# Performance work log

Hardware: AMD Instinct MI355X
Metric: run time of the kernel (lower is better)

The kernel has to match this reference:

```python
import jax, jax.numpy as jnp
import numpy as np

B, S, HID = 4, 4096, 1024
H, D = 16, 64  # num_head, attn_dim
EPS = 1e-6


def setup_inputs() -> dict:
    key = jax.random.key(0)
    ks = jax.random.split(key, 9)
    sc = 1.0 / np.sqrt(HID)
    return {
        "x": jax.random.normal(ks[0], (B, S, HID), jnp.float32),
        "Wq": jax.random.normal(ks[1], (HID, H * D), jnp.float32) * sc,
        "bq": jnp.zeros((H * D,), jnp.float32),
        "Wk": jax.random.normal(ks[2], (HID, H * D), jnp.float32) * sc,
        "bk": jnp.zeros((H * D,), jnp.float32),
        "Wv": jax.random.normal(ks[3], (HID, H * D), jnp.float32) * sc,
        "bv": jnp.zeros((H * D,), jnp.float32),
        "Wo": jax.random.normal(ks[4], (H * D, HID), jnp.float32) * sc,
        "bo": jnp.zeros((HID,), jnp.float32),
    }


def _phi(x):
    # feature_map == 'elu': elu(x) + 1
    return jax.nn.elu(x) + 1.0


def reference(x, Wq, bq, Wk, bk, Wv, bv, Wo, bo):
    bs, n, _ = x.shape
    # projections -> [b, n, h, d], then scan axis first -> [n, b, h, d]
    Q = _phi((x @ Wq + bq).reshape(bs, n, H, D)).transpose(1, 0, 2, 3)
    K = _phi((x @ Wk + bk).reshape(bs, n, H, D)).transpose(1, 0, 2, 3)
    V = (x @ Wv + bv).reshape(bs, n, H, D).transpose(1, 0, 2, 3)

    KV0 = jnp.zeros((bs, H, D, D), x.dtype)
    Ks0 = jnp.zeros((bs, H, D), x.dtype)

    def step(carry, qkv):
        KV, Ks = carry
        qi, ki, vi = qkv  # each [b, h, d]
        KV = KV + jnp.einsum('bhd,bhe->bhde', ki, vi)
        Ks = Ks + ki
        num = jnp.einsum('bhd,bhde->bhe', qi, KV)
        den = jnp.einsum('bhd,bhd->bh', qi, Ks)
        return (KV, Ks), num / (den[..., None] + EPS)

    _, out = jax.lax.scan(step, (KV0, Ks0), (Q, K, V))  # out: [n, b, h, d]
    out = out.transpose(1, 0, 2, 3).reshape(bs, n, H * D)
    return out @ Wo + bo
```

## Files before the change

kernel.cpp:

```cpp
#include <hip/hip_runtime.h>
#include <stdint.h>


#define DEVI __device__ __forceinline__

typedef __attribute__((ext_vector_type(8))) short bf16x8;
typedef __attribute__((ext_vector_type(4))) float f32x4;
typedef unsigned short u16;

DEVI u16 f2bf(float f) {
  union { float f; uint32_t u; } x; x.f = f;
  return (u16)((x.u + 0x7FFFu + ((x.u >> 16) & 1u)) >> 16);
}
DEVI float bf2f(u16 u) {
  union { uint32_t u; float f; } x; x.u = ((uint32_t)u) << 16;
  return x.f;
}
DEVI f32x4 mfma16(bf16x8 a, bf16x8 b, f32x4 c) {
  return __builtin_amdgcn_mfma_f32_16x16x32_bf16(a, b, c, 0, 0, 0);
}

typedef __attribute__((address_space(3))) void* lds_vp;
typedef const __attribute__((address_space(1))) void* glb_vp;
DEVI void gload_lds16(const void* g, void* l) {
  __builtin_amdgcn_global_load_lds((glb_vp)g, (lds_vp)l, 16, 0, 0);
}

static constexpr int Ss  = 4096;
static constexpr int Hh  = 16;
static constexpr int CC  = 64;
static constexpr int NCC = Ss / CC;

__global__ __launch_bounds__(256) void cvt_bf16_k(const float* __restrict__ in,
                                                  u16* __restrict__ out, int n8) {
  const int i = blockIdx.x * 256 + threadIdx.x;
  if (i >= n8) return;
  const float4* p = (const float4*)(in + (size_t)i * 8);
  const float4 a = p[0], b = p[1];
  union { uint4 v; u16 s[8]; } u;
  u.s[0] = f2bf(a.x); u.s[1] = f2bf(a.y); u.s[2] = f2bf(a.z); u.s[3] = f2bf(a.w);
  u.s[4] = f2bf(b.x); u.s[5] = f2bf(b.y); u.s[6] = f2bf(b.z); u.s[7] = f2bf(b.w);
  ((uint4*)out)[i] = u.v;
}

__global__ __launch_bounds__(256) void transpose_cvt_k(const float* __restrict__ in,
                                                       u16* __restrict__ out) {
  __shared__ float tl[32][33];
  const int tx = threadIdx.x & 31, ty = threadIdx.x >> 5;
  const int bx = blockIdx.x, by = blockIdx.y;
#pragma unroll
  for (int j = 0; j < 4; ++j)
    tl[ty + j * 8][tx] = in[(size_t)(by * 32 + ty + j * 8) * 1024 + bx * 32 + tx];
  __syncthreads();
#pragma unroll
  for (int j = 0; j < 4; ++j)
    out[(size_t)(bx * 32 + ty + j * 8) * 1024 + by * 32 + tx] = f2bf(tl[tx][ty + j * 8]);
}

template <bool FUSED, bool OUTF32>
__global__ __launch_bounds__(512, 2) void gemm256_k(const u16* __restrict__ A,
                                                    const u16* __restrict__ BT,
                                                    const float* __restrict__ b0,
                                                    const float* __restrict__ b1,
                                                    const float* __restrict__ b2,
                                                    void* __restrict__ out,
                                                    int M, int K) {
  __shared__ __attribute__((aligned(16))) u16 lds[65536];
  const int t = threadIdx.x, lane = t & 63, w = t >> 6;
  const int wm = w >> 2, wn = w & 3;

  const int nx = gridDim.x;
  const int nwg = nx * gridDim.y;
  const int bid = blockIdx.y * nx + blockIdx.x;
  const int swz = (bid & 7) * (nwg >> 3) + (bid >> 3);
  const int bx = swz % nx, by = swz / nx;
  const int m0 = by * 256, n0 = bx * 256;

  const u16* gA = A + (size_t)m0 * K;
  const u16* gB = BT + (size_t)n0 * K;

  const int sr = t >> 2;
  const int sc = (t & 3) ^ ((sr >> 1) & 3);
  auto stage = [&](const u16* gm, u16* dst, int kof) {
    gload_lds16(gm + (size_t)sr * K + kof + sc * 8, dst + t * 8);
    gload_lds16(gm + (size_t)(sr + 128) * K + kof + sc * 8, dst + 4096 + t * 8);
  };

  f32x4 acc[8][4];
#pragma unroll
  for (int i = 0; i < 8; ++i)
#pragma unroll
    for (int j = 0; j < 4; ++j) acc[i][j] = f32x4{0.f, 0.f, 0.f, 0.f};

  stage(gA, lds, 0);          stage(gB, lds + 32768, 0);
  stage(gA, lds + 8192, 32);  stage(gB, lds + 40960, 32);

  const int fr = lane & 15, kq = lane >> 4;
  const int rdko = ((kq ^ ((fr >> 1) & 3)) << 3);
  const int arow0 = wm * 128 + fr;
  const int brow0 = wn * 64 + fr;

  const int nk = K >> 6;
  for (int kt = 0; kt < nk; ++kt) {
    const int buf = kt & 1;
    u16* Ax = lds + buf * 16384;
    u16* Bx = lds + 32768 + buf * 16384;
    u16* Ay = lds + (buf ^ 1) * 16384;
    u16* By = lds + 32768 + (buf ^ 1) * 16384;
    const bool pf = (kt + 1 < nk);
    const int kon = (kt + 1) << 6;
    bf16x8 af[8], bg0, bg1;

#pragma unroll
    for (int half = 0; half < 2; ++half) {
      u16* Axh = Ax + half * 8192;
      u16* Bxh = Bx + half * 8192;
      if (half == 0 || pf) asm volatile("s_waitcnt vmcnt(4)" ::: "memory");
      else                 asm volatile("s_waitcnt vmcnt(0)" ::: "memory");
      __builtin_amdgcn_s_barrier();
      if (pf) stage(gA, Ay + half * 8192, kon + half * 32);
#pragma unroll
      for (int fi = 0; fi < 8; ++fi)
        af[fi] = *(const bf16x8*)(Axh + (arow0 + fi * 16) * 32 + rdko);
      bg0 = *(const bf16x8*)(Bxh + brow0 * 32 + rdko);
      bg1 = *(const bf16x8*)(Bxh + (brow0 + 16) * 32 + rdko);
      asm volatile("s_waitcnt lgkmcnt(0)" ::: "memory");
      __builtin_amdgcn_sched_barrier(0);
      __builtin_amdgcn_s_setprio(1);
#pragma unroll
      for (int fi = 0; fi < 8; ++fi) {
        acc[fi][0] = mfma16(af[fi], bg0, acc[fi][0]);
        acc[fi][1] = mfma16(af[fi], bg1, acc[fi][1]);
      }
      __builtin_amdgcn_s_setprio(0);
      __builtin_amdgcn_sched_barrier(0);
      if (pf) stage(gB, By + half * 8192, kon + half * 32);
      bg0 = *(const bf16x8*)(Bxh + (brow0 + 32) * 32 + rdko);
      bg1 = *(const bf16x8*)(Bxh + (brow0 + 48) * 32 + rdko);
      asm volatile("s_waitcnt lgkmcnt(0)" ::: "memory");
      __builtin_amdgcn_sched_barrier(0);
      __builtin_amdgcn_s_setprio(1);
#pragma unroll
      for (int fi = 0; fi < 8; ++fi) {
        acc[fi][2] = mfma16(af[fi], bg0, acc[fi][2]);
        acc[fi][3] = mfma16(af[fi], bg1, acc[fi][3]);
      }
      __builtin_amdgcn_s_setprio(0);
      __builtin_amdgcn_sched_barrier(0);
    }
  }

  const int rowg = (lane >> 4) * 4;
  if constexpr (!OUTF32) {
    __syncthreads();
    const int seg  = FUSED ? (n0 >> 10) : 0;
    const int lcol0 = FUSED ? (n0 & 1023) : n0;
    const float* bp = b0;
    if constexpr (FUSED) bp = (seg == 0) ? b0 : (seg == 1) ? b1 : b2;
#pragma unroll
    for (int fj = 0; fj < 4; ++fj) {
      const int col = wn * 64 + fj * 16 + fr;
      const float bv = bp[lcol0 + col];
#pragma unroll
      for (int fi = 0; fi < 8; ++fi) {
#pragma unroll
        for (int rr = 0; rr < 4; ++rr) {
          const int row = wm * 128 + fi * 16 + rowg + rr;
          float v = acc[fi][fj][rr] + bv;
          if (FUSED && seg < 2) v = (v > 0.f) ? (v + 1.f) : __expf(v);
          lds[row * 256 + (((col >> 3) ^ ((row >> 2) & 31)) << 3) + (col & 7)] = f2bf(v);
        }
      }
    }
    __syncthreads();
    u16* outp = (u16*)out + (size_t)seg * M * 1024 + (size_t)m0 * 1024 + lcol0;
#pragma unroll
    for (int it = 0; it < 16; ++it) {
      const int g = it * 512 + t;
      const int row = g >> 5, c16 = g & 31;
      const uint4 v = *(const uint4*)&lds[row * 256 + ((c16 ^ ((row >> 2) & 31)) << 3)];
      *(uint4*)(outp + (size_t)row * 1024 + c16 * 8) = v;
    }
  } else {
    float* flds = (float*)lds;
#pragma unroll
    for (int pass = 0; pass < 2; ++pass) {
      __syncthreads();
      if (wm == pass) {
#pragma unroll
        for (int fj = 0; fj < 4; ++fj) {
          const int col = wn * 64 + fj * 16 + fr;
          const float bv = b0[n0 + col];
#pragma unroll
          for (int fi = 0; fi < 8; ++fi) {
#pragma unroll
            for (int rr = 0; rr < 4; ++rr) {
              const int rl = fi * 16 + rowg + rr;
              flds[rl * 256 + (((col >> 2) ^ ((rl >> 2) & 63)) << 2) + (col & 3)] =
                  acc[fi][fj][rr] + bv;
            }
          }
        }
      }
      __syncthreads();
      float* outp = (float*)out + (size_t)(m0 + pass * 128) * 1024 + n0;
#pragma unroll
      for (int it = 0; it < 16; ++it) {
        const int g = it * 512 + t;
        const int row = g >> 6, c16 = g & 63;
        const uint4 v = *(const uint4*)&flds[row * 256 + ((c16 ^ ((row >> 2) & 63)) << 2)];
        *(uint4*)(outp + (size_t)row * 1024 + c16 * 4) = v;
      }
    }
  }
}

__global__ __launch_bounds__(256) void chunk_kv_k(const u16* __restrict__ Kb,
                                                  const u16* __restrict__ Vb,
                                                  u16* __restrict__ KVTc,
                                                  float* __restrict__ Ksc) {
  const int c = blockIdx.x, h = blockIdx.y, b = blockIdx.z;
  __shared__ u16 KT[64][72], VT[64][72];
  const int t = threadIdx.x, lane = t & 63, w = t >> 6;
  {
    const int i = t >> 2, c0 = (t & 3) * 16;
    const size_t g = ((size_t)(b * Ss + c * CC + i)) * 1024 + h * 64 + c0;
    const u16* kp = Kb + g;
    const u16* vp = Vb + g;
#pragma unroll
    for (int j = 0; j < 16; ++j) { KT[c0 + j][i] = kp[j]; VT[c0 + j][i] = vp[j]; }
  }
  __syncthreads();
  f32x4 acc[4];
#pragma unroll
  for (int j = 0; j < 4; ++j) acc[j] = f32x4{0.f, 0.f, 0.f, 0.f};
  const int fr = lane & 15, kq = (lane >> 4) * 8;
#pragma unroll
  for (int kk = 0; kk < 2; ++kk) {
    const bf16x8 av = *(const bf16x8*)&VT[w * 16 + fr][kk * 32 + kq];
#pragma unroll
    for (int fj = 0; fj < 4; ++fj) {
      const bf16x8 bk = *(const bf16x8*)&KT[fj * 16 + fr][kk * 32 + kq];
      acc[fj] = mfma16(av, bk, acc[fj]);
    }
  }
  const size_t base = ((size_t)((b * Hh + h) * NCC + c)) * 4096;
#pragma unroll
  for (int fj = 0; fj < 4; ++fj)
#pragma unroll
    for (int rr = 0; rr < 4; ++rr) {
      const int e = w * 16 + (lane >> 4) * 4 + rr;
      const int d = fj * 16 + fr;
      KVTc[base + (size_t)e * 64 + d] = f2bf(acc[fj][rr]);
    }
  if (t < 64) {
    float s = 0.f;
#pragma unroll
    for (int ii = 0; ii < 8; ++ii) {
      const bf16x8 kv = *(const bf16x8*)&KT[t][ii * 8];
#pragma unroll
      for (int j = 0; j < 8; ++j) s += bf2f((u16)kv[j]);
    }
    Ksc[((size_t)((b * Hh + h) * NCC + c)) * 64 + t] = s;
  }
}

__global__ __launch_bounds__(256) void prefix_k(const u16* __restrict__ KVTc,
                                                const float* __restrict__ Ksc,
                                                u16* __restrict__ KVpreT,
                                                float* __restrict__ Kspre) {
  const int bh = blockIdx.x, eg = blockIdx.y;
  const int t = threadIdx.x;
  const int e4 = eg * 1024 + t * 4;
  const u16* src = KVTc + (size_t)bh * NCC * 4096 + e4;
  u16* dst = KVpreT + (size_t)bh * NCC * 4096 + e4;
  const float* kss = Ksc + (size_t)bh * NCC * 64 + t;
  float* ksd = Kspre + (size_t)bh * NCC * 64 + t;
  float run[4] = {0.f, 0.f, 0.f, 0.f};
  float rk = 0.f;
  for (int c = 0; c < NCC; ++c) {
    union { uint2 v; u16 s[4]; } in, ov;
    in.v = *(const uint2*)(src + (size_t)c * 4096);
#pragma unroll
    for (int j = 0; j < 4; ++j) { ov.s[j] = f2bf(run[j]); run[j] += bf2f(in.s[j]); }
    *(uint2*)(dst + (size_t)c * 4096) = ov.v;
    if (eg == 0 && t < 64) { ksd[(size_t)c * 64] = rk; rk += kss[(size_t)c * 64]; }
  }
}

__global__ __launch_bounds__(256) void chunk_out_k(const u16* __restrict__ Qb,
                                                   const u16* __restrict__ Kb,
                                                   const u16* __restrict__ Vb,
                                                   const u16* __restrict__ KVpreT,
                                                   const float* __restrict__ Kspre,
                                                   u16* __restrict__ attn) {
  const int c = blockIdx.x, h = blockIdx.y, b = blockIdx.z;
  const int bh = b * Hh + h;
  __shared__ u16 Ql[64][72], Kl[64][72], VT[64][72], Pl[64][72];
  __shared__ float den[64];
  const int t = threadIdx.x, lane = t & 63, w = t >> 6;

  {
    const int i = t >> 2, c0 = (t & 3) * 16;
    const size_t g = ((size_t)(b * Ss + c * CC + i)) * 1024 + h * 64 + c0;
    const uint4* qp = (const uint4*)(Qb + g);
    uint4* qd = (uint4*)&Ql[i][c0]; qd[0] = qp[0]; qd[1] = qp[1];
    const uint4* kp = (const uint4*)(Kb + g);
    uint4* kd = (uint4*)&Kl[i][c0]; kd[0] = kp[0]; kd[1] = kp[1];
    const u16* vp = Vb + g;
#pragma unroll
    for (int j = 0; j < 16; ++j) VT[c0 + j][i] = vp[j];
  }
  __syncthreads();

  f32x4 sacc[4];
#pragma unroll
  for (int fj = 0; fj < 4; ++fj) sacc[fj] = f32x4{0.f, 0.f, 0.f, 0.f};
#pragma unroll
  for (int kd = 0; kd < 2; ++kd) {
    const bf16x8 aq = *(const bf16x8*)&Ql[w * 16 + (lane & 15)][kd * 32 + (lane >> 4) * 8];
#pragma unroll
    for (int fj = 0; fj < 4; ++fj) {
      const bf16x8 bk = *(const bf16x8*)&Kl[fj * 16 + (lane & 15)][kd * 32 + (lane >> 4) * 8];
      sacc[fj] = mfma16(aq, bk, sacc[fj]);
    }
  }
  float rowsum[4] = {0.f, 0.f, 0.f, 0.f};
#pragma unroll
  for (int fj = 0; fj < 4; ++fj) {
#pragma unroll
    for (int rr = 0; rr < 4; ++rr) {
      const int i_loc = w * 16 + (lane >> 4) * 4 + rr;
      const int j_loc = fj * 16 + (lane & 15);
      const float v = (j_loc <= i_loc) ? sacc[fj][rr] : 0.f;
      Pl[i_loc][j_loc] = f2bf(v);
      rowsum[rr] += v;
    }
  }
#pragma unroll
  for (int off = 1; off < 16; off <<= 1) {
#pragma unroll
    for (int rr = 0; rr < 4; ++rr) rowsum[rr] += __shfl_xor(rowsum[rr], off, 64);
  }
  if ((lane & 15) == 0) {
#pragma unroll
    for (int rr = 0; rr < 4; ++rr) den[w * 16 + (lane >> 4) * 4 + rr] = rowsum[rr];
  }
  __syncthreads();
  {
    const int i = t >> 2, part = t & 3;
    const float* ksp = Kspre + ((size_t)(bh * NCC + c)) * 64 + part * 16;
    float s = 0.f;
#pragma unroll
    for (int sg = 0; sg < 2; ++sg) {
      const bf16x8 q = *(const bf16x8*)&Ql[i][part * 16 + sg * 8];
#pragma unroll
      for (int j = 0; j < 8; ++j) s += bf2f((u16)q[j]) * ksp[sg * 8 + j];
    }
    s += __shfl_xor(s, 1, 64);
    s += __shfl_xor(s, 2, 64);
    if (part == 0) den[i] = den[i] + s + 1e-6f;
  }
  __syncthreads();

  f32x4 oacc[4];
#pragma unroll
  for (int fj = 0; fj < 4; ++fj) oacc[fj] = f32x4{0.f, 0.f, 0.f, 0.f};
  const u16* kvb = KVpreT + ((size_t)(bh * NCC + c)) * 4096;
#pragma unroll
  for (int ks2 = 0; ks2 < 2; ++ks2) {
    const bf16x8 aq = *(const bf16x8*)&Ql[w * 16 + (lane & 15)][ks2 * 32 + (lane >> 4) * 8];
#pragma unroll
    for (int fj = 0; fj < 4; ++fj) {
      const bf16x8 bv =
          *(const bf16x8*)(kvb + (size_t)(fj * 16 + (lane & 15)) * 64 + ks2 * 32 + (lane >> 4) * 8);
      oacc[fj] = mfma16(aq, bv, oacc[fj]);
    }
  }
#pragma unroll
  for (int ks3 = 0; ks3 < 2; ++ks3) {
    const bf16x8 ap = *(const bf16x8*)&Pl[w * 16 + (lane & 15)][ks3 * 32 + (lane >> 4) * 8];
#pragma unroll
    for (int fj = 0; fj < 4; ++fj) {
      const bf16x8 bv = *(const bf16x8*)&VT[fj * 16 + (lane & 15)][ks3 * 32 + (lane >> 4) * 8];
      oacc[fj] = mfma16(ap, bv, oacc[fj]);
    }
  }
#pragma unroll
  for (int fj = 0; fj < 4; ++fj) {
#pragma unroll
    for (int rr = 0; rr < 4; ++rr) {
      const int i_loc = w * 16 + (lane >> 4) * 4 + rr;
      const int e = fj * 16 + (lane & 15);
      const float v = oacc[fj][rr] / den[i_loc];
      attn[((size_t)(b * Ss + c * CC + i_loc)) * 1024 + h * 64 + e] = f2bf(v);
    }
  }
}

extern "C" void kernel_launch(void* const* d_in, const int* in_sizes, int n_in,
                              void* d_out, int out_size, void* d_ws, size_t ws_size,
                              hipStream_t stream) {
  (void)in_sizes; (void)n_in; (void)out_size; (void)ws_size;
  const float* x  = (const float*)d_in[0];
  const float* Wq = (const float*)d_in[1];
  const float* bq = (const float*)d_in[2];
  const float* Wk = (const float*)d_in[3];
  const float* bk = (const float*)d_in[4];
  const float* Wv = (const float*)d_in[5];
  const float* bv = (const float*)d_in[6];
  const float* Wo = (const float*)d_in[7];
  const float* bo = (const float*)d_in[8];
  float* out = (float*)d_out;
  char* ws = (char*)d_ws;

  size_t off = 0;
  auto take = [&](size_t bytes) { size_t r = off; off += (bytes + 255) & ~(size_t)255; return r; };
  const size_t WQKV_B = (size_t)3072 * 1024 * 2;
  const size_t WT_B   = (size_t)1024 * 1024 * 2;
  const size_t BIG_B  = (size_t)16384 * 1024 * 2;
  const size_t KVT_B  = (size_t)64 * NCC * 4096 * 2;
  const size_t KS_B   = (size_t)64 * NCC * 64 * 4;

  u16* WqkvT  = (u16*)(ws + take(WQKV_B));
  u16* WoT    = (u16*)(ws + take(WT_B));
  size_t shared_off = take(BIG_B);
  u16* xbf    = (u16*)(ws + shared_off);
  u16* KVTc   = (u16*)(ws + shared_off);
  u16* attn   = (u16*)(ws + shared_off);
  u16* Qb     = (u16*)(ws + take(BIG_B));
  u16* Kb     = (u16*)(ws + take(BIG_B));
  u16* Vb     = (u16*)(ws + take(BIG_B));
  u16* KVpreT = (u16*)(ws + take(KVT_B));
  float* Ksc  = (float*)(ws + take(KS_B));
  float* Kspre= (float*)(ws + take(KS_B));

  const dim3 blk(256);
  cvt_bf16_k<<<dim3(8192), blk, 0, stream>>>(x, xbf, 16384 * 1024 / 8);
  const dim3 gT(32, 32);
  transpose_cvt_k<<<gT, blk, 0, stream>>>(Wq, WqkvT);
  transpose_cvt_k<<<gT, blk, 0, stream>>>(Wk, WqkvT + (size_t)1024 * 1024);
  transpose_cvt_k<<<gT, blk, 0, stream>>>(Wv, WqkvT + (size_t)2048 * 1024);
  transpose_cvt_k<<<gT, blk, 0, stream>>>(Wo, WoT);

  gemm256_k<true, false><<<dim3(12, 64), dim3(512), 0, stream>>>(
      xbf, WqkvT, bq, bk, bv, Qb, 16384, 1024);

  const dim3 gC(NCC, Hh, 4);
  chunk_kv_k<<<gC, blk, 0, stream>>>(Kb, Vb, KVTc, Ksc);
  prefix_k<<<dim3(64, 4), blk, 0, stream>>>(KVTc, Ksc, KVpreT, Kspre);
  chunk_out_k<<<gC, blk, 0, stream>>>(Qb, Kb, Vb, KVpreT, Kspre, attn);

  gemm256_k<false, true><<<dim3(4, 64), dim3(512), 0, stream>>>(
      attn, WoT, bo, NULL, NULL, out, 16384, 1024);
}
```

Before: 267.4 us.

## Restructure GEMM barrier/prefetch schedule and merge four weight-transpose launches

```diff
diff --git a/kernel.cpp b/kernel.cpp
--- a/kernel.cpp
+++ b/kernel.cpp
@@ -25,6 +25,10 @@
 DEVI void gload_lds16(const void* g, void* l) {
   __builtin_amdgcn_global_load_lds((glb_vp)g, (lds_vp)l, 16, 0, 0);
 }
+
+#define BAR()   asm volatile("s_barrier" ::: "memory")
+#define LGKM0() do { asm volatile("s_waitcnt lgkmcnt(0)" ::: "memory"); \
+                     __builtin_amdgcn_sched_barrier(0); } while (0)
 
 static constexpr int Ss  = 4096;
 static constexpr int Hh  = 16;
@@ -43,9 +47,16 @@
   ((uint4*)out)[i] = u.v;
 }
 
-__global__ __launch_bounds__(256) void transpose_cvt_k(const float* __restrict__ in,
-                                                       u16* __restrict__ out) {
+__global__ __launch_bounds__(256) void transpose_cvt4_k(const float* __restrict__ w0,
+                                                        const float* __restrict__ w1,
+                                                        const float* __restrict__ w2,
+                                                        const float* __restrict__ w3,
+                                                        u16* __restrict__ dqkv,
+                                                        u16* __restrict__ dwo) {
   __shared__ float tl[32][33];
+  const int z = blockIdx.z;
+  const float* in = (z == 0) ? w0 : (z == 1) ? w1 : (z == 2) ? w2 : w3;
+  u16* out = (z < 3) ? (dqkv + (size_t)z * 1024 * 1024) : dwo;
   const int tx = threadIdx.x & 31, ty = threadIdx.x >> 5;
   const int bx = blockIdx.x, by = blockIdx.y;
 #pragma unroll
@@ -94,6 +105,8 @@
 
   stage(gA, lds, 0);          stage(gB, lds + 32768, 0);
   stage(gA, lds + 8192, 32);  stage(gB, lds + 40960, 32);
+  asm volatile("s_waitcnt vmcnt(4)" ::: "memory");
+  BAR();
 
   const int fr = lane & 15, kq = lane >> 4;
   const int rdko = ((kq ^ ((fr >> 1) & 3)) << 3);
@@ -102,30 +115,26 @@
 
   const int nk = K >> 6;
   for (int kt = 0; kt < nk; ++kt) {
-    const int buf = kt & 1;
-    u16* Ax = lds + buf * 16384;
-    u16* Bx = lds + 32768 + buf * 16384;
-    u16* Ay = lds + (buf ^ 1) * 16384;
-    u16* By = lds + 32768 + (buf ^ 1) * 16384;
+    const int d = kt & 1;
     const bool pf = (kt + 1 < nk);
     const int kon = (kt + 1) << 6;
+    u16* Ac = lds + d * 16384;
+    u16* Bc = lds + 32768 + d * 16384;
+    u16* An = lds + (d ^ 1) * 16384;
+    u16* Bn = lds + 32768 + (d ^ 1) * 16384;
     bf16x8 af[8], bg0, bg1;
-
-#pragma unroll
-    for (int half = 0; half < 2; ++half) {
-      u16* Axh = Ax + half * 8192;
-      u16* Bxh = Bx + half * 8192;
-      if (half == 0 || pf) asm volatile("s_waitcnt vmcnt(4)" ::: "memory");
-      else                 asm volatile("s_waitcnt vmcnt(0)" ::: "memory");
-      __builtin_amdgcn_s_barrier();
-      if (pf) stage(gA, Ay + half * 8192, kon + half * 32);
+#pragma unroll
+    for (int h = 0; h < 2; ++h) {
+      const u16* Ah = Ac + h * 8192;
+      const u16* Bh = Bc + h * 8192;
 #pragma unroll
       for (int fi = 0; fi < 8; ++fi)
-        af[fi] = *(const bf16x8*)(Axh + (arow0 + fi * 16) * 32 + rdko);
-      bg0 = *(const bf16x8*)(Bxh + brow0 * 32 + rdko);
-      bg1 = *(const bf16x8*)(Bxh + (brow0 + 16) * 32 + rdko);
-      asm volatile("s_waitcnt lgkmcnt(0)" ::: "memory");
-      __builtin_amdgcn_sched_barrier(0);
+        af[fi] = *(const bf16x8*)(Ah + (arow0 + fi * 16) * 32 + rdko);
+      bg0 = *(const bf16x8*)(Bh + brow0 * 32 + rdko);
+      bg1 = *(const bf16x8*)(Bh + (brow0 + 16) * 32 + rdko);
+      if (pf) stage(gA, An + h * 8192, kon + h * 32);
+      BAR();
+      LGKM0();
       __builtin_amdgcn_s_setprio(1);
 #pragma unroll
       for (int fi = 0; fi < 8; ++fi) {
@@ -134,11 +143,12 @@
       }
       __builtin_amdgcn_s_setprio(0);
       __builtin_amdgcn_sched_barrier(0);
-      if (pf) stage(gB, By + half * 8192, kon + half * 32);
-      bg0 = *(const bf16x8*)(Bxh + (brow0 + 32) * 32 + rdko);
-      bg1 = *(const bf16x8*)(Bxh + (brow0 + 48) * 32 + rdko);
-      asm volatile("s_waitcnt lgkmcnt(0)" ::: "memory");
-      __builtin_amdgcn_sched_barrier(0);
+      BAR();
+      bg0 = *(const bf16x8*)(Bh + (brow0 + 32) * 32 + rdko);
+      bg1 = *(const bf16x8*)(Bh + (brow0 + 48) * 32 + rdko);
+      if (pf) stage(gB, Bn + h * 8192, kon + h * 32);
+      BAR();
+      LGKM0();
       __builtin_amdgcn_s_setprio(1);
 #pragma unroll
       for (int fi = 0; fi < 8; ++fi) {
@@ -147,6 +157,13 @@
       }
       __builtin_amdgcn_s_setprio(0);
       __builtin_amdgcn_sched_barrier(0);
+      if (h == 0) {
+        if (pf) asm volatile("s_waitcnt vmcnt(4)" ::: "memory");
+        else    asm volatile("s_waitcnt vmcnt(0)" ::: "memory");
+      } else if (pf) {
+        asm volatile("s_waitcnt vmcnt(4)" ::: "memory");
+      }
+      BAR();
     }
   }
 
@@ -437,11 +454,7 @@
 
   const dim3 blk(256);
   cvt_bf16_k<<<dim3(8192), blk, 0, stream>>>(x, xbf, 16384 * 1024 / 8);
-  const dim3 gT(32, 32);
-  transpose_cvt_k<<<gT, blk, 0, stream>>>(Wq, WqkvT);
-  transpose_cvt_k<<<gT, blk, 0, stream>>>(Wk, WqkvT + (size_t)1024 * 1024);
-  transpose_cvt_k<<<gT, blk, 0, stream>>>(Wv, WqkvT + (size_t)2048 * 1024);
-  transpose_cvt_k<<<gT, blk, 0, stream>>>(Wo, WoT);
+  transpose_cvt4_k<<<dim3(32, 32, 4), blk, 0, stream>>>(Wq, Wk, Wv, Wo, WqkvT, WoT);
 
   gemm256_k<true, false><<<dim3(12, 64), dim3(512), 0, stream>>>(
       xbf, WqkvT, bq, bk, bv, Qb, 16384, 1024);
```

New measurement: 266.3 us. No clear change (-0.4%).

## Fuse chunked linear attention into one sequential-scan kernel per head slice

Applied to the files above, without the earlier changes.

```diff
diff --git a/kernel.cpp b/kernel.cpp
--- a/kernel.cpp
+++ b/kernel.cpp
@@ -25,6 +25,9 @@
 DEVI void gload_lds16(const void* g, void* l) {
   __builtin_amdgcn_global_load_lds((glb_vp)g, (lds_vp)l, 16, 0, 0);
 }
+
+#define LGKM_BAR() do { asm volatile("s_waitcnt lgkmcnt(0)" ::: "memory"); \
+                        __builtin_amdgcn_s_barrier(); } while (0)
 
 static constexpr int Ss  = 4096;
 static constexpr int Hh  = 16;
@@ -43,9 +46,16 @@
   ((uint4*)out)[i] = u.v;
 }
 
-__global__ __launch_bounds__(256) void transpose_cvt_k(const float* __restrict__ in,
-                                                       u16* __restrict__ out) {
+__global__ __launch_bounds__(256) void transpose_cvt4_k(const float* __restrict__ w0,
+                                                        const float* __restrict__ w1,
+                                                        const float* __restrict__ w2,
+                                                        const float* __restrict__ w3,
+                                                        u16* __restrict__ dqkv,
+                                                        u16* __restrict__ dwo) {
   __shared__ float tl[32][33];
+  const int z = blockIdx.z;
+  const float* in = (z == 0) ? w0 : (z == 1) ? w1 : (z == 2) ? w2 : w3;
+  u16* out = (z < 3) ? (dqkv + (size_t)z * 1024 * 1024) : dwo;
   const int tx = threadIdx.x & 31, ty = threadIdx.x >> 5;
   const int bx = blockIdx.x, by = blockIdx.y;
 #pragma unroll
@@ -215,186 +225,155 @@
   }
 }
 
-__global__ __launch_bounds__(256) void chunk_kv_k(const u16* __restrict__ Kb,
-                                                  const u16* __restrict__ Vb,
-                                                  u16* __restrict__ KVTc,
-                                                  float* __restrict__ Ksc) {
-  const int c = blockIdx.x, h = blockIdx.y, b = blockIdx.z;
-  __shared__ u16 KT[64][72], VT[64][72];
+__global__ __launch_bounds__(512, 1) void fused_attn_k(const u16* __restrict__ Qb,
+                                                       const u16* __restrict__ Kb,
+                                                       const u16* __restrict__ Vb,
+                                                       u16* __restrict__ attn) {
+  __shared__ __attribute__((aligned(16))) u16 Ql[2][4096];
+  __shared__ u16 Kl[64][72], KTl[64][72];
+  __shared__ u16 VT[16][72], KVbf[16][72];
+  __shared__ u16 Pl[64][72];
+  __shared__ float Ksf[64], ksp[4][64], denp[2][64], den[64];
+
   const int t = threadIdx.x, lane = t & 63, w = t >> 6;
-  {
-    const int i = t >> 2, c0 = (t & 3) * 16;
-    const size_t g = ((size_t)(b * Ss + c * CC + i)) * 1024 + h * 64 + c0;
-    const u16* kp = Kb + g;
-    const u16* vp = Vb + g;
-#pragma unroll
-    for (int j = 0; j < 16; ++j) { KT[c0 + j][i] = kp[j]; VT[c0 + j][i] = vp[j]; }
-  }
-  __syncthreads();
-  f32x4 acc[4];
-#pragma unroll
-  for (int j = 0; j < 4; ++j) acc[j] = f32x4{0.f, 0.f, 0.f, 0.f};
-  const int fr = lane & 15, kq = (lane >> 4) * 8;
-#pragma unroll
-  for (int kk = 0; kk < 2; ++kk) {
-    const bf16x8 av = *(const bf16x8*)&VT[w * 16 + fr][kk * 32 + kq];
-#pragma unroll
-    for (int fj = 0; fj < 4; ++fj) {
-      const bf16x8 bk = *(const bf16x8*)&KT[fj * 16 + fr][kk * 32 + kq];
-      acc[fj] = mfma16(av, bk, acc[fj]);
-    }
-  }
-  const size_t base = ((size_t)((b * Hh + h) * NCC + c)) * 4096;
-#pragma unroll
-  for (int fj = 0; fj < 4; ++fj)
-#pragma unroll
-    for (int rr = 0; rr < 4; ++rr) {
-      const int e = w * 16 + (lane >> 4) * 4 + rr;
-      const int d = fj * 16 + fr;
-      KVTc[base + (size_t)e * 64 + d] = f2bf(acc[fj][rr]);
-    }
-  if (t < 64) {
-    float s = 0.f;
-#pragma unroll
-    for (int ii = 0; ii < 8; ++ii) {
-      const bf16x8 kv = *(const bf16x8*)&KT[t][ii * 8];
-#pragma unroll
-      for (int j = 0; j < 8; ++j) s += bf2f((u16)kv[j]);
-    }
-    Ksc[((size_t)((b * Hh + h) * NCC + c)) * 64 + t] = s;
-  }
-}
-
-__global__ __launch_bounds__(256) void prefix_k(const u16* __restrict__ KVTc,
-                                                const float* __restrict__ Ksc,
-                                                u16* __restrict__ KVpreT,
-                                                float* __restrict__ Kspre) {
-  const int bh = blockIdx.x, eg = blockIdx.y;
-  const int t = threadIdx.x;
-  const int e4 = eg * 1024 + t * 4;
-  const u16* src = KVTc + (size_t)bh * NCC * 4096 + e4;
-  u16* dst = KVpreT + (size_t)bh * NCC * 4096 + e4;
-  const float* kss = Ksc + (size_t)bh * NCC * 64 + t;
-  float* ksd = Kspre + (size_t)bh * NCC * 64 + t;
-  float run[4] = {0.f, 0.f, 0.f, 0.f};
-  float rk = 0.f;
+  const int bid = blockIdx.x;
+  const int g = bid & 7, slot = bid >> 3;
+  const int bh = g * 8 + (slot >> 2), eg = slot & 3;
+  const int b = bh >> 4, h = bh & 15;
+
+  const u16* qbase = Qb + (size_t)(b * Ss) * 1024 + h * 64;
+  const u16* kbase = Kb + (size_t)(b * Ss) * 1024 + h * 64;
+  const u16* vbase = Vb + (size_t)(b * Ss) * 1024 + h * 64 + eg * 16;
+  u16* abase = attn + (size_t)(b * Ss) * 1024 + h * 64 + eg * 16;
+
+  const int qr = t >> 3, qc = t & 7;
+  const int kr = t >> 3, kc8 = (t & 7) * 8;
+  const int vr = t >> 3, vc = (t & 7) * 2;
+  const int fr = lane & 15, kq = lane >> 4;
+
+  auto qstage = [&](int c, int buf) {
+    gload_lds16(qbase + (size_t)(c * 64 + qr) * 1024 + ((qc ^ (qr & 7)) << 3),
+                &Ql[buf][t * 8]);
+  };
+  uint4 kreg; uint32_t vreg;
+  auto kvload = [&](int c) {
+    kreg = *(const uint4*)(kbase + (size_t)(c * 64 + kr) * 1024 + kc8);
+    vreg = *(const uint32_t*)(vbase + (size_t)(c * 64 + vr) * 1024 + vc);
+  };
+
+  f32x4 kvacc = f32x4{0.f, 0.f, 0.f, 0.f};
+  if (t < 64) Ksf[t] = 0.f;
+
+  qstage(0, 0);
+  kvload(0);
+
   for (int c = 0; c < NCC; ++c) {
-    union { uint2 v; u16 s[4]; } in, ov;
-    in.v = *(const uint2*)(src + (size_t)c * 4096);
-#pragma unroll
-    for (int j = 0; j < 4; ++j) { ov.s[j] = f2bf(run[j]); run[j] += bf2f(in.s[j]); }
-    *(uint2*)(dst + (size_t)c * 4096) = ov.v;
-    if (eg == 0 && t < 64) { ksd[(size_t)c * 64] = rk; rk += kss[(size_t)c * 64]; }
-  }
-}
-
-__global__ __launch_bounds__(256) void chunk_out_k(const u16* __restrict__ Qb,
-                                                   const u16* __restrict__ Kb,
-                                                   const u16* __restrict__ Vb,
-                                                   const u16* __restrict__ KVpreT,
-                                                   const float* __restrict__ Kspre,
-                                                   u16* __restrict__ attn) {
-  const int c = blockIdx.x, h = blockIdx.y, b = blockIdx.z;
-  const int bh = b * Hh + h;
-  __shared__ u16 Ql[64][72], Kl[64][72], VT[64][72], Pl[64][72];
-  __shared__ float den[64];
-  const int t = threadIdx.x, lane = t & 63, w = t >> 6;
-
-  {
-    const int i = t >> 2, c0 = (t & 3) * 16;
-    const size_t g = ((size_t)(b * Ss + c * CC + i)) * 1024 + h * 64 + c0;
-    const uint4* qp = (const uint4*)(Qb + g);
-    uint4* qd = (uint4*)&Ql[i][c0]; qd[0] = qp[0]; qd[1] = qp[1];
-    const uint4* kp = (const uint4*)(Kb + g);
-    uint4* kd = (uint4*)&Kl[i][c0]; kd[0] = kp[0]; kd[1] = kp[1];
-    const u16* vp = Vb + g;
-#pragma unroll
-    for (int j = 0; j < 16; ++j) VT[c0 + j][i] = vp[j];
-  }
-  __syncthreads();
-
-  f32x4 sacc[4];
-#pragma unroll
-  for (int fj = 0; fj < 4; ++fj) sacc[fj] = f32x4{0.f, 0.f, 0.f, 0.f};
-#pragma unroll
-  for (int kd = 0; kd < 2; ++kd) {
-    const bf16x8 aq = *(const bf16x8*)&Ql[w * 16 + (lane & 15)][kd * 32 + (lane >> 4) * 8];
-#pragma unroll
-    for (int fj = 0; fj < 4; ++fj) {
-      const bf16x8 bk = *(const bf16x8*)&Kl[fj * 16 + (lane & 15)][kd * 32 + (lane >> 4) * 8];
-      sacc[fj] = mfma16(aq, bk, sacc[fj]);
-    }
-  }
-  float rowsum[4] = {0.f, 0.f, 0.f, 0.f};
-#pragma unroll
-  for (int fj = 0; fj < 4; ++fj) {
-#pragma unroll
-    for (int rr = 0; rr < 4; ++rr) {
-      const int i_loc = w * 16 + (lane >> 4) * 4 + rr;
-      const int j_loc = fj * 16 + (lane & 15);
-      const float v = (j_loc <= i_loc) ? sacc[fj][rr] : 0.f;
-      Pl[i_loc][j_loc] = f2bf(v);
-      rowsum[rr] += v;
-    }
-  }
-#pragma unroll
-  for (int off = 1; off < 16; off <<= 1) {
-#pragma unroll
-    for (int rr = 0; rr < 4; ++rr) rowsum[rr] += __shfl_xor(rowsum[rr], off, 64);
-  }
-  if ((lane & 15) == 0) {
-#pragma unroll
-    for (int rr = 0; rr < 4; ++rr) den[w * 16 + (lane >> 4) * 4 + rr] = rowsum[rr];
-  }
-  __syncthreads();
-  {
-    const int i = t >> 2, part = t & 3;
-    const float* ksp = Kspre + ((size_t)(bh * NCC + c)) * 64 + part * 16;
-    float s = 0.f;
-#pragma unroll
-    for (int sg = 0; sg < 2; ++sg) {
-      const bf16x8 q = *(const bf16x8*)&Ql[i][part * 16 + sg * 8];
-#pragma unroll
-      for (int j = 0; j < 8; ++j) s += bf2f((u16)q[j]) * ksp[sg * 8 + j];
-    }
-    s += __shfl_xor(s, 1, 64);
-    s += __shfl_xor(s, 2, 64);
-    if (part == 0) den[i] = den[i] + s + 1e-6f;
-  }
-  __syncthreads();
-
-  f32x4 oacc[4];
-#pragma unroll
-  for (int fj = 0; fj < 4; ++fj) oacc[fj] = f32x4{0.f, 0.f, 0.f, 0.f};
-  const u16* kvb = KVpreT + ((size_t)(bh * NCC + c)) * 4096;
-#pragma unroll
-  for (int ks2 = 0; ks2 < 2; ++ks2) {
-    const bf16x8 aq = *(const bf16x8*)&Ql[w * 16 + (lane & 15)][ks2 * 32 + (lane >> 4) * 8];
-#pragma unroll
-    for (int fj = 0; fj < 4; ++fj) {
-      const bf16x8 bv =
-          *(const bf16x8*)(kvb + (size_t)(fj * 16 + (lane & 15)) * 64 + ks2 * 32 + (lane >> 4) * 8);
-      oacc[fj] = mfma16(aq, bv, oacc[fj]);
-    }
-  }
-#pragma unroll
-  for (int ks3 = 0; ks3 < 2; ++ks3) {
-    const bf16x8 ap = *(const bf16x8*)&Pl[w * 16 + (lane & 15)][ks3 * 32 + (lane >> 4) * 8];
-#pragma unroll
-    for (int fj = 0; fj < 4; ++fj) {
-      const bf16x8 bv = *(const bf16x8*)&VT[fj * 16 + (lane & 15)][ks3 * 32 + (lane >> 4) * 8];
-      oacc[fj] = mfma16(ap, bv, oacc[fj]);
-    }
-  }
-#pragma unroll
-  for (int fj = 0; fj < 4; ++fj) {
-#pragma unroll
-    for (int rr = 0; rr < 4; ++rr) {
-      const int i_loc = w * 16 + (lane >> 4) * 4 + rr;
-      const int e = fj * 16 + (lane & 15);
-      const float v = oacc[fj][rr] / den[i_loc];
-      attn[((size_t)(b * Ss + c * CC + i_loc)) * 1024 + h * 64 + e] = f2bf(v);
-    }
+    const int buf = c & 1;
+    {
+      union { uint4 v; u16 s[8]; } ku; ku.v = kreg;
+      *(uint4*)&Kl[kr][kc8] = ku.v;
+#pragma unroll
+      for (int j = 0; j < 8; ++j) KTl[kc8 + j][kr] = ku.s[j];
+      union { uint32_t v; u16 s[2]; } vu; vu.v = vreg;
+      VT[vc][vr] = vu.s[0]; VT[vc + 1][vr] = vu.s[1];
+      if (w >= 4) {
+#pragma unroll
+        for (int r = 0; r < 4; ++r)
+          KVbf[(lane >> 4) * 4 + r][(w - 4) * 16 + fr] = f2bf(kvacc[r]);
+      }
+    }
+    if (c + 1 < NCC) { qstage(c + 1, buf ^ 1); kvload(c + 1); }
+    LGKM_BAR();
+
+    const int r0 = (w & 3) * 16;
+    const int ch = w >> 2;
+    f32x4 sacc[2];
+    sacc[0] = f32x4{0.f, 0.f, 0.f, 0.f};
+    sacc[1] = f32x4{0.f, 0.f, 0.f, 0.f};
+#pragma unroll
+    for (int kk = 0; kk < 2; ++kk) {
+      const bf16x8 aq =
+          *(const bf16x8*)&Ql[buf][(r0 + fr) * 64 + (((kk * 4 + kq) ^ (fr & 7)) << 3)];
+#pragma unroll
+      for (int j = 0; j < 2; ++j) {
+        const bf16x8 bk = *(const bf16x8*)&Kl[(ch * 2 + j) * 16 + fr][kk * 32 + kq * 8];
+        sacc[j] = mfma16(aq, bk, sacc[j]);
+      }
+    }
+    float rs[4] = {0.f, 0.f, 0.f, 0.f};
+#pragma unroll
+    for (int j = 0; j < 2; ++j) {
+      const int colb = (ch * 2 + j) * 16 + fr;
+#pragma unroll
+      for (int rr = 0; rr < 4; ++rr) {
+        const int i_loc = r0 + (lane >> 4) * 4 + rr;
+        const float v = (colb <= i_loc) ? sacc[j][rr] : 0.f;
+        Pl[i_loc][colb] = f2bf(v);
+        rs[rr] += v;
+      }
+    }
+#pragma unroll
+    for (int off = 1; off < 16; off <<= 1)
+#pragma unroll
+      for (int rr = 0; rr < 4; ++rr) rs[rr] += __shfl_xor(rs[rr], off, 64);
+    if ((lane & 15) == 0) {
+#pragma unroll
+      for (int rr = 0; rr < 4; ++rr) denp[ch][r0 + (lane >> 4) * 4 + rr] = rs[rr];
+    }
+    if (w < 4) {
+      float kp = 0.f;
+#pragma unroll
+      for (int i = 0; i < 16; ++i) kp += bf2f(Kl[w * 16 + i][lane]);
+      ksp[w][lane] = kp;
+    }
+    LGKM_BAR();
+
+    if (t < 256) {
+      const int i = t >> 2, part = t & 3;
+      float s = 0.f;
+#pragma unroll
+      for (int sg = 0; sg < 2; ++sg) {
+        const int cnk = part * 2 + sg;
+        const bf16x8 q = *(const bf16x8*)&Ql[buf][i * 64 + ((cnk ^ (i & 7)) << 3)];
+#pragma unroll
+        for (int j2 = 0; j2 < 8; ++j2) s += bf2f((u16)q[j2]) * Ksf[part * 16 + sg * 8 + j2];
+      }
+      s += __shfl_xor(s, 1, 64);
+      s += __shfl_xor(s, 2, 64);
+      if (part == 0) den[i] = denp[0][i] + denp[1][i] + s + 1e-6f;
+    }
+    LGKM_BAR();
+
+    if (w < 4) {
+      f32x4 oacc = f32x4{0.f, 0.f, 0.f, 0.f};
+#pragma unroll
+      for (int kk = 0; kk < 2; ++kk) {
+        const bf16x8 aq =
+            *(const bf16x8*)&Ql[buf][(w * 16 + fr) * 64 + (((kk * 4 + kq) ^ (fr & 7)) << 3)];
+        const bf16x8 bkv = *(const bf16x8*)&KVbf[fr][kk * 32 + kq * 8];
+        oacc = mfma16(aq, bkv, oacc);
+      }
+#pragma unroll
+      for (int kk = 0; kk < 2; ++kk) {
+        const bf16x8 ap = *(const bf16x8*)&Pl[w * 16 + fr][kk * 32 + kq * 8];
+        const bf16x8 bv = *(const bf16x8*)&VT[fr][kk * 32 + kq * 8];
+        oacc = mfma16(ap, bv, oacc);
+      }
+#pragma unroll
+      for (int r = 0; r < 4; ++r) {
+        const int i_loc = w * 16 + (lane >> 4) * 4 + r;
+        abase[(size_t)(c * 64 + i_loc) * 1024 + fr] = f2bf(oacc[r] / den[i_loc]);
+      }
+      if (t < 64) Ksf[t] += ksp[0][t] + ksp[1][t] + ksp[2][t] + ksp[3][t];
+    } else {
+#pragma unroll
+      for (int kk = 0; kk < 2; ++kk) {
+        const bf16x8 av = *(const bf16x8*)&VT[fr][kk * 32 + kq * 8];
+        const bf16x8 bk2 = *(const bf16x8*)&KTl[(w - 4) * 16 + fr][kk * 32 + kq * 8];
+        kvacc = mfma16(av, bk2, kvacc);
+      }
+    }
+    LGKM_BAR();
   }
 }
 
@@ -419,37 +398,24 @@
   const size_t WQKV_B = (size_t)3072 * 1024 * 2;
   const size_t WT_B   = (size_t)1024 * 1024 * 2;
   const size_t BIG_B  = (size_t)16384 * 1024 * 2;
-  const size_t KVT_B  = (size_t)64 * NCC * 4096 * 2;
-  const size_t KS_B   = (size_t)64 * NCC * 64 * 4;
 
   u16* WqkvT  = (u16*)(ws + take(WQKV_B));
   u16* WoT    = (u16*)(ws + take(WT_B));
   size_t shared_off = take(BIG_B);
   u16* xbf    = (u16*)(ws + shared_off);
-  u16* KVTc   = (u16*)(ws + shared_off);
   u16* attn   = (u16*)(ws + shared_off);
   u16* Qb     = (u16*)(ws + take(BIG_B));
   u16* Kb     = (u16*)(ws + take(BIG_B));
   u16* Vb     = (u16*)(ws + take(BIG_B));
-  u16* KVpreT = (u16*)(ws + take(KVT_B));
-  float* Ksc  = (float*)(ws + take(KS_B));
-  float* Kspre= (float*)(ws + take(KS_B));
 
   const dim3 blk(256);
   cvt_bf16_k<<<dim3(8192), blk, 0, stream>>>(x, xbf, 16384 * 1024 / 8);
-  const dim3 gT(32, 32);
-  transpose_cvt_k<<<gT, blk, 0, stream>>>(Wq, WqkvT);
-  transpose_cvt_k<<<gT, blk, 0, stream>>>(Wk, WqkvT + (size_t)1024 * 1024);
-  transpose_cvt_k<<<gT, blk, 0, stream>>>(Wv, WqkvT + (size_t)2048 * 1024);
-  transpose_cvt_k<<<gT, blk, 0, stream>>>(Wo, WoT);
+  transpose_cvt4_k<<<dim3(32, 32, 4), blk, 0, stream>>>(Wq, Wk, Wv, Wo, WqkvT, WoT);
 
   gemm256_k<true, false><<<dim3(12, 64), dim3(512), 0, stream>>>(
       xbf, WqkvT, bq, bk, bv, Qb, 16384, 1024);
 
-  const dim3 gC(NCC, Hh, 4);
-  chunk_kv_k<<<gC, blk, 0, stream>>>(Kb, Vb, KVTc, Ksc);
-  prefix_k<<<dim3(64, 4), blk, 0, stream>>>(KVTc, Ksc, KVpreT, Kspre);
-  chunk_out_k<<<gC, blk, 0, stream>>>(Qb, Kb, Vb, KVpreT, Kspre, attn);
+  fused_attn_k<<<dim3(256), dim3(512), 0, stream>>>(Qb, Kb, Vb, attn);
 
   gemm256_k<false, true><<<dim3(4, 64), dim3(512), 0, stream>>>(
       attn, WoT, bo, NULL, NULL, out, 16384, 1024);
```

Result: slower. 320.6 us (+19.9%).
